# Kernel optimization log

Measured on AMD Instinct MI355X. Metric: run time of the kernel, lower is better.

Reference implementation:

```python
import jax, jax.numpy as jnp
import numpy as np

EPS = 1e-6

def masked_softmax(x, m, axis):
    # Faithful to KrantikariQA tensor_utils.masked_softmax:
    #   x = x*m; e = exp(x - max(x)) * m; e / (sum(e) + 1e-6)
    x = x * m
    ex = jnp.exp(x - jnp.max(x, axis=axis, keepdims=True)) * m
    return ex / (jnp.sum(ex, axis=axis, keepdims=True) + EPS)

def setup_inputs() -> dict:
    key = jax.random.key(0)
    k = jax.random.split(key, 7)
    Lq, Lp, B, D = 256, 256, 64, 1024
    q = jax.random.normal(k[0], (Lq, B, D), jnp.float32)
    p = jax.random.normal(k[1], (Lp, B, D), jnp.float32)
    qm = jax.random.randint(k[2], (B, Lq), 0, 2).astype(jnp.int32)
    pm = jax.random.randint(k[3], (B, Lp), 0, 2).astype(jnp.int32)
    # nn.Linear weights (out, in), no bias
    WF = jax.random.normal(k[4], (D, D), jnp.float32) * 0.02
    WG = jax.random.normal(k[5], (D, 2 * D), jnp.float32) * 0.02
    WH = jax.random.normal(k[6], (1, 2 * D), jnp.float32) * 0.02
    return {"q": q, "p": p, "qm": qm, "pm": pm, "WF": WF, "WG": WG, "WH": WH}

def reference(q, p, qm, pm, WF, WG, WH):
    # Attend: att = F(x), batch-first [B, L, D]
    att_q = jnp.einsum('lbd,ed->ble', q, WF)          # [B,Lq,D]
    att_p = jnp.einsum('lbd,ed->ble', p, WF)          # [B,Lp,D]
    e = jnp.einsum('bqe,bpe->bqp', att_q, att_p)      # [B,Lq,Lp]
    m = qm.astype(q.dtype)[:, :, None] * pm.astype(q.dtype)[:, None, :]  # [B,Lq,Lp]
    softmax_j = masked_softmax(e, m, axis=2)                              # over Lp
    softmax_i = masked_softmax(e.transpose(0, 2, 1), m.transpose(0, 2, 1), axis=2)  # [B,Lp,Lq]
    beta = jnp.einsum('bqp,pbd->bqd', softmax_j, p)   # [B,Lq,D]
    alpha = jnp.einsum('bpq,qbd->bpd', softmax_i, q)  # [B,Lp,D]
    # Compare
    v1 = jnp.concatenate([q.transpose(1, 0, 2), beta], axis=-1) @ WG.T   # [B,Lq,D]
    v2 = jnp.concatenate([p.transpose(1, 0, 2), alpha], axis=-1) @ WG.T  # [B,Lp,D]
    # Aggregate
    sum_v1 = jnp.sum(v1, axis=1)  # [B,D]
    sum_v2 = jnp.sum(v2, axis=1)  # [B,D]
    return jnp.concatenate([sum_v1, sum_v2], axis=-1) @ WH.T  # [B,1]
```

## Files before the change

kernel.cpp:

```cpp
#include <hip/hip_runtime.h>

typedef _Float16 f16x8 __attribute__((ext_vector_type(8)));
using f32x4 = __attribute__((ext_vector_type(4))) float;

constexpr int B = 64, L = 256, D = 1024;
constexpr int BD = B * D;
constexpr float EPS = 1e-6f;

__device__ __forceinline__ void gload_lds16(const void* g, void* l) {
    __builtin_amdgcn_global_load_lds((const __attribute__((address_space(1))) void*)g,
                                     (__attribute__((address_space(3))) void*)l,
                                     16, 0, 0);
}

__global__ __launch_bounds__(256) void k_cvt(const float* __restrict__ x,
                                             short* __restrict__ y) {
    const int i = blockIdx.x * 256 + threadIdx.x;
    const float4* xp = (const float4*)x;
    float4 a = xp[2 * i], b = xp[2 * i + 1];
    float v[8] = {a.x, a.y, a.z, a.w, b.x, b.y, b.z, b.w};
    union { _Float16 h[8]; int4 q; } u;
    #pragma unroll
    for (int k = 0; k < 8; ++k) u.h[k] = (_Float16)v[k];
    ((int4*)y)[i] = u.q;
}

__global__ __launch_bounds__(256) void k_cvt_t(const float* __restrict__ X,
                                               short* __restrict__ Y) {
    __shared__ float tile[32][33];
    const int t = threadIdx.x;
    const int rt = blockIdx.y, ct = blockIdx.x;
    const int r = t >> 3, c4 = (t & 7) * 4;
    float4 v = *(const float4*)(X + (long)(rt * 32 + r) * D + ct * 32 + c4);
    tile[r][c4] = v.x; tile[r][c4 + 1] = v.y; tile[r][c4 + 2] = v.z; tile[r][c4 + 3] = v.w;
    __syncthreads();
    union { _Float16 h[4]; short4 s; } u;
    u.h[0] = (_Float16)tile[c4 + 0][r];
    u.h[1] = (_Float16)tile[c4 + 1][r];
    u.h[2] = (_Float16)tile[c4 + 2][r];
    u.h[3] = (_Float16)tile[c4 + 3][r];
    *(short4*)(Y + (long)(ct * 32 + r) * D + rt * 32 + c4) = u.s;
}

__global__ __launch_bounds__(256, 4) void k_gemm16(
    const short* __restrict__ A, long strideA, long batchA,
    const short* __restrict__ Bm, long strideB, long batchB,
    int K, int bx, int per_batch, int f16_out,
    short* __restrict__ Ch, float* __restrict__ Cf, int ldC, long batchC)
{
    __shared__ __align__(16) short lds_s[16384];
    const int t = threadIdx.x, lane = t & 63, w = t >> 6;
    const int wm = w >> 1, wn = w & 1;

    const int lin = blockIdx.x;
    const int chunk = gridDim.x >> 3;
    const int swz = (lin & 7) * chunk + (lin >> 3);
    const int z = swz / per_batch;
    const int r0 = swz % per_batch;
    const int mb = (r0 / bx) * 128, nb = (r0 % bx) * 128;

    const char* mat = (w < 2) ? ((const char*)A + batchA * z)
                              : ((const char*)Bm + batchB * z);
    const long rstride = (w < 2) ? strideA : strideB;
    const int row0 = (w < 2) ? mb : nb;
    const int half = (w & 1) * 64;
    const char* sp[4];
    #pragma unroll
    for (int i = 0; i < 4; ++i) {
        int tr = half + i * 16 + (lane >> 2);
        int g = (lane & 3) ^ ((tr >> 1) & 3);
        sp[i] = mat + (long)(row0 + tr) * rstride + g * 16;
    }
    short* dst0 = lds_s + ((w >> 1) ? 4096 : 0) + (w & 1) * 2048;

    int aoff[4], boff[4];
    #pragma unroll
    for (int f = 0; f < 4; ++f) {
        int ra = wm * 64 + f * 16 + (lane & 15);
        aoff[f] = (ra * 4 + ((lane >> 4) ^ ((ra >> 1) & 3))) * 16;
        int rb = wn * 64 + f * 16 + (lane & 15);
        boff[f] = 8192 + (rb * 4 + ((lane >> 4) ^ ((rb >> 1) & 3))) * 16;
    }

    f32x4 acc[4][4] = {};
    const int NT = K >> 5;

    {
        #pragma unroll
        for (int i = 0; i < 4; ++i) gload_lds16(sp[i], dst0 + i * 512);
    }
    __syncthreads();

    int cur = 0;
    for (int kt = 0; kt < NT; ++kt) {
        if (kt + 1 < NT) {
            short* dst = dst0 + (cur ^ 1) * 8192;
            long ko = (long)(kt + 1) * 64;
            #pragma unroll
            for (int i = 0; i < 4; ++i) gload_lds16(sp[i] + ko, dst + i * 512);
        }
        const char* lb = (const char*)lds_s + cur * 16384;
        f16x8 a[4], b[4];
        #pragma unroll
        for (int f = 0; f < 4; ++f) {
            a[f] = *(const f16x8*)(lb + aoff[f]);
            b[f] = *(const f16x8*)(lb + boff[f]);
        }
        #pragma unroll
        for (int i = 0; i < 4; ++i)
            #pragma unroll
            for (int j = 0; j < 4; ++j)
                acc[i][j] = __builtin_amdgcn_mfma_f32_16x16x32_f16(b[j], a[i], acc[i][j], 0, 0, 0);
        __syncthreads();
        cur ^= 1;
    }

    const long zC = batchC * z;
    #pragma unroll
    for (int i = 0; i < 4; ++i)
        #pragma unroll
        for (int j = 0; j < 4; ++j) {
            int row = mb + wm * 64 + i * 16 + (lane & 15);
            int col = nb + wn * 64 + j * 16 + (lane >> 4) * 4;
            long idx = zC + (long)row * ldC + col;
            if (f16_out) {
                union { _Float16 h[4]; short4 s; } u;
                #pragma unroll
                for (int rr = 0; rr < 4; ++rr) u.h[rr] = (_Float16)acc[i][j][rr];
                *(short4*)(Ch + idx) = u.s;
            } else {
                float4 v = make_float4(acc[i][j][0], acc[i][j][1], acc[i][j][2], acc[i][j][3]);
                *(float4*)(Cf + idx) = v;
            }
        }
}

__global__ __launch_bounds__(256) void k_pass1(const float* __restrict__ E,
                                               const int* __restrict__ qm,
                                               const int* __restrict__ pm,
                                               float* __restrict__ impart,
                                               float* __restrict__ ispart,
                                               float* __restrict__ cjpart) {
    const int qc = blockIdx.x, b = blockIdx.y;
    const int p = threadIdx.x, lane = p & 63, w = p >> 6;
    const int q0 = qc * 32;
    __shared__ float wred[32][4];
    __shared__ float rowmx[32], rowsm[32], qmv_s[32];
    if (p < 32) qmv_s[p] = (float)qm[b * L + q0 + p];
    __syncthreads();
    const float pmv = (float)pm[b * L + p];
    const float* eb = E + b * (L * L) + q0 * L + p;

    float xv[32];
    float im = -1e30f;
    #pragma unroll
    for (int r = 0; r < 32; ++r) {
        float mm = pmv * qmv_s[r];
        float x = eb[r * L] * mm;
        xv[r] = x;
        im = fmaxf(im, x);
        float v = x;
        #pragma unroll
        for (int o = 32; o; o >>= 1) v = fmaxf(v, __shfl_xor(v, o));
        if (lane == 0) wred[r][w] = v;
    }
    __syncthreads();
    if (p < 32) rowmx[p] = fmaxf(fmaxf(wred[p][0], wred[p][1]), fmaxf(wred[p][2], wred[p][3]));
    __syncthreads();
    float is = 0.f;
    #pragma unroll
    for (int r = 0; r < 32; ++r) {
        float mm = pmv * qmv_s[r];
        is += mm * __expf(xv[r] - im);
        float v = mm * __expf(xv[r] - rowmx[r]);
        #pragma unroll
        for (int o = 32; o; o >>= 1) v += __shfl_xor(v, o);
        if (lane == 0) wred[r][w] = v;
    }
    __syncthreads();
    if (p < 32) rowsm[p] = wred[p][0] + wred[p][1] + wred[p][2] + wred[p][3];
    __syncthreads();
    float cj = 0.f;
    #pragma unroll
    for (int r = 0; r < 32; ++r) {
        float mm = pmv * qmv_s[r];
        cj += mm * __expf(xv[r] - rowmx[r]) / (rowsm[r] + EPS);
    }
    const int o = (b * 8 + qc) * 256 + p;
    impart[o] = im; ispart[o] = is; cjpart[o] = cj;
}

__global__ __launch_bounds__(256) void k_combine(const float* __restrict__ impart,
                                                 const float* __restrict__ ispart,
                                                 const float* __restrict__ cjpart,
                                                 float* __restrict__ rmi,
                                                 float* __restrict__ rsi,
                                                 float* __restrict__ colj) {
    const int b = blockIdx.x, p = threadIdx.x;
    const int base = b * 8 * 256 + p;
    float m = -1e30f, s = 0.f, c = 0.f;
    #pragma unroll
    for (int k = 0; k < 8; ++k) m = fmaxf(m, impart[base + k * 256]);
    #pragma unroll
    for (int k = 0; k < 8; ++k) {
        s += ispart[base + k * 256] * __expf(impart[base + k * 256] - m);
        c += cjpart[base + k * 256];
    }
    rmi[b * L + p] = m; rsi[b * L + p] = s; colj[b * L + p] = c;
}

__global__ __launch_bounds__(256) void k_colsum_i(const float* __restrict__ E,
                                                  const int* __restrict__ qm,
                                                  const int* __restrict__ pm,
                                                  const float* __restrict__ rmaxi,
                                                  const float* __restrict__ rsumi,
                                                  float* __restrict__ coli) {
    const int wid = threadIdx.x >> 6, lane = threadIdx.x & 63;
    const int row = blockIdx.x * 4 + wid;
    const int b = row >> 8;
    const float qmv = (float)qm[row];
    const float* er = E + row * L;
    float acc = 0.f;
    #pragma unroll
    for (int i = 0; i < 4; ++i) {
        int pp = lane + 64 * i;
        float mm = qmv * (float)pm[b * L + pp];
        float x = er[pp] * mm;
        acc += mm * __expf(x - rmaxi[b * L + pp]) / (rsumi[b * L + pp] + EPS);
    }
    #pragma unroll
    for (int o = 32; o; o >>= 1) acc += __shfl_xor(acc, o);
    if (lane == 0) coli[row] = acc;
}

__global__ __launch_bounds__(256) void k_sums(const short* __restrict__ Q16,
                                              const short* __restrict__ P16,
                                              const float* __restrict__ colj,
                                              const float* __restrict__ coli,
                                              float* __restrict__ sumq,
                                              float* __restrict__ sump,
                                              float* __restrict__ sumbeta,
                                              float* __restrict__ sumalpha) {
    const int b = blockIdx.x >> 2;
    const int d = (blockIdx.x & 3) * 256 + threadIdx.x;
    const _Float16* Q = (const _Float16*)Q16;
    const _Float16* P = (const _Float16*)P16;
    float aq = 0.f, ap = 0.f, ab = 0.f, aa = 0.f;
    for (int l = 0; l < L; ++l) {
        float qv = (float)Q[(long)l * BD + b * D + d];
        float pv = (float)P[(long)l * BD + b * D + d];
        aq += qv; ap += pv;
        ab += colj[b * L + l] * pv;
        aa += coli[b * L + l] * qv;
    }
    sumq[b * D + d] = aq;  sump[b * D + d] = ap;
    sumbeta[b * D + d] = ab; sumalpha[b * D + d] = aa;
}

__global__ __launch_bounds__(256) void k_gpart(const float* __restrict__ WG,
                                               const float* __restrict__ WH,
                                               float* __restrict__ gp1,
                                               float* __restrict__ gp2) {
    const int k = blockIdx.x * 256 + threadIdx.x;
    const int e0 = blockIdx.y * 128;
    float a = 0.f, c = 0.f;
    for (int e = 0; e < 128; ++e) {
        float w = WG[(long)(e0 + e) * (2 * D) + k];
        a += w * WH[e0 + e];
        c += w * WH[D + e0 + e];
    }
    gp1[blockIdx.y * 2048 + k] = a; gp2[blockIdx.y * 2048 + k] = c;
}

__global__ __launch_bounds__(256) void k_final(const float* __restrict__ sumq,
                                               const float* __restrict__ sump,
                                               const float* __restrict__ sumbeta,
                                               const float* __restrict__ sumalpha,
                                               const float* __restrict__ gp1,
                                               const float* __restrict__ gp2,
                                               float* __restrict__ out) {
    const int b = blockIdx.x, t = threadIdx.x;
    float acc = 0.f;
    for (int d = t; d < D; d += 256) {
        float g1d = 0.f, g1D = 0.f, g2d = 0.f, g2D = 0.f;
        #pragma unroll
        for (int ec = 0; ec < 8; ++ec) {
            g1d += gp1[ec * 2048 + d];     g1D += gp1[ec * 2048 + D + d];
            g2d += gp2[ec * 2048 + d];     g2D += gp2[ec * 2048 + D + d];
        }
        acc += sumq[b * D + d] * g1d + sumbeta[b * D + d] * g1D +
               sump[b * D + d] * g2d + sumalpha[b * D + d] * g2D;
    }
    #pragma unroll
    for (int o = 32; o; o >>= 1) acc += __shfl_xor(acc, o);
    __shared__ float red[4];
    const int wid = t >> 6, lane = t & 63;
    if (lane == 0) red[wid] = acc;
    __syncthreads();
    if (t == 0) out[b] = red[0] + red[1] + red[2] + red[3];
}

extern "C" void kernel_launch(void* const* d_in, const int* in_sizes, int n_in,
                              void* d_out, int out_size, void* d_ws, size_t ws_size,
                              hipStream_t stream) {
    const float* q  = (const float*)d_in[0];
    const float* p  = (const float*)d_in[1];
    const int*   qm = (const int*)d_in[2];
    const int*   pm = (const int*)d_in[3];
    const float* WF = (const float*)d_in[4];
    const float* WG = (const float*)d_in[5];
    const float* WH = (const float*)d_in[6];
    float* out = (float*)d_out;

    char* wsb = (char*)d_ws;
    short* q16   = (short*)(wsb);
    short* p16   = (short*)(wsb + (32l << 20));
    short* T16   = (short*)(wsb + (64l << 20));
    short* WFt16 = (short*)(wsb + (96l << 20));
    short* G16   = (short*)(wsb + (98l << 20));
    float* E     = (float*)(wsb + (100l << 20));
    float* st    = (float*)(wsb + (116l << 20));
    const int BL = B * L;
    float* impart = st;                 float* ispart = impart + B * 8 * 256;
    float* cjpart = ispart + B * 8 * 256;
    float* rmi  = cjpart + B * 8 * 256; float* rsi  = rmi + BL;
    float* colj = rsi + BL;             float* coli = colj + BL;
    float* sumq = coli + BL;            float* sump = sumq + B * D;
    float* sumb = sump + B * D;         float* suma = sumb + B * D;
    float* gp1  = suma + B * D;         float* gp2  = gp1 + 8 * 2048;

    k_cvt<<<8192, 256, 0, stream>>>(q, q16);
    k_cvt<<<8192, 256, 0, stream>>>(p, p16);
    k_cvt_t<<<dim3(32, 32), 256, 0, stream>>>(WF, WFt16);
    k_gemm16<<<64, 256, 0, stream>>>(WFt16, 2048, 0, WFt16, 2048, 0,
                                     1024, 8, 64, 1, G16, nullptr, 1024, 0);
    k_gemm16<<<1024, 256, 0, stream>>>(q16, 2048, 0, G16, 2048, 0,
                                       1024, 8, 1024, 1, T16, nullptr, 1024, 0);
    k_gemm16<<<256, 256, 0, stream>>>(T16, 64l * 2048, 2048, p16, 64l * 2048, 2048,
                                      1024, 2, 4, 0, nullptr, E, 256, 65536);
    k_pass1<<<dim3(8, B), 256, 0, stream>>>(E, qm, pm, impart, ispart, cjpart);
    k_combine<<<B, 256, 0, stream>>>(impart, ispart, cjpart, rmi, rsi, colj);
    k_colsum_i<<<BL / 4, 256, 0, stream>>>(E, qm, pm, rmi, rsi, coli);
    k_sums<<<B * 4, 256, 0, stream>>>(q16, p16, colj, coli, sumq, sump, sumb, suma);
    k_gpart<<<dim3(8, 8), 256, 0, stream>>>(WG, WH, gp1, gp2);
    k_final<<<B, 256, 0, stream>>>(sumq, sump, sumb, suma, gp1, gp2, out);
}
```

Baseline: 195.8 us.

## Templatize GEMM tiles, split-K WF^T WF, fuse conversions, split-L reduction sums

Replaces the fixed 128x128 GEMM with a templated version supporting different warp layouts, including a 256x256 tile for the big q·G GEMM. The GEMM also gets a single-barrier-per-iteration pipeline. The small WF^T·WF GEMM becomes a 4-way split-K with a fold kernel, giving more blocks. The q/p conversions are merged into one launch. The column-sum kernel is split over four L chunks with 8-wide vector loads, with the chunks reduced in the final kernel. This adds partial buffers and an extra fold launch.

```diff
diff --git a/kernel.cpp b/kernel.cpp
--- a/kernel.cpp
+++ b/kernel.cpp
@@ -13,16 +13,21 @@
                                      16, 0, 0);
 }
 
-__global__ __launch_bounds__(256) void k_cvt(const float* __restrict__ x,
-                                             short* __restrict__ y) {
+__global__ __launch_bounds__(256) void k_cvt2(const float* __restrict__ q,
+                                              const float* __restrict__ p,
+                                              short* __restrict__ q16,
+                                              short* __restrict__ p16) {
     const int i = blockIdx.x * 256 + threadIdx.x;
-    const float4* xp = (const float4*)x;
-    float4 a = xp[2 * i], b = xp[2 * i + 1];
+    constexpr int HALF = (L * B * D) / 8;
+    const float* src; short* dst; int j;
+    if (i < HALF) { src = q; dst = q16; j = i; }
+    else          { src = p; dst = p16; j = i - HALF; }
+    float4 a = ((const float4*)src)[2 * j], b = ((const float4*)src)[2 * j + 1];
     float v[8] = {a.x, a.y, a.z, a.w, b.x, b.y, b.z, b.w};
-    union { _Float16 h[8]; int4 q; } u;
+    union { _Float16 h[8]; int4 q4; } u;
     #pragma unroll
     for (int k = 0; k < 8; ++k) u.h[k] = (_Float16)v[k];
-    ((int4*)y)[i] = u.q;
+    ((int4*)dst)[j] = u.q4;
 }
 
 __global__ __launch_bounds__(256) void k_cvt_t(const float* __restrict__ X,
@@ -42,85 +47,97 @@
     *(short4*)(Y + (long)(ct * 32 + r) * D + rt * 32 + c4) = u.s;
 }
 
-__global__ __launch_bounds__(256, 4) void k_gemm16(
-    const short* __restrict__ A, long strideA, long batchA,
-    const short* __restrict__ Bm, long strideB, long batchB,
+template <int WM, int WN, int MR>
+__global__ __launch_bounds__(WM * WN * 64) void k_gemm(
+    const short* __restrict__ A, long sA, long bA,
+    const short* __restrict__ Bm, long sB, long bB,
     int K, int bx, int per_batch, int f16_out,
     short* __restrict__ Ch, float* __restrict__ Cf, int ldC, long batchC)
 {
-    __shared__ __align__(16) short lds_s[16384];
+    constexpr int BM = WM * MR * 16, BN = WN * 64;
+    constexpr int T = WM * WN * 64;
+    constexpr int TILEB = (BM + BN) * 64;
+    constexpr int ROUNDS = TILEB / (T * 16);
+    __shared__ __align__(16) char lds[2 * TILEB];
+
     const int t = threadIdx.x, lane = t & 63, w = t >> 6;
-    const int wm = w >> 1, wn = w & 1;
+    const int wm = w / WN, wn = w % WN;
 
     const int lin = blockIdx.x;
     const int chunk = gridDim.x >> 3;
     const int swz = (lin & 7) * chunk + (lin >> 3);
     const int z = swz / per_batch;
     const int r0 = swz % per_batch;
-    const int mb = (r0 / bx) * 128, nb = (r0 % bx) * 128;
-
-    const char* mat = (w < 2) ? ((const char*)A + batchA * z)
-                              : ((const char*)Bm + batchB * z);
-    const long rstride = (w < 2) ? strideA : strideB;
-    const int row0 = (w < 2) ? mb : nb;
-    const int half = (w & 1) * 64;
-    const char* sp[4];
-    #pragma unroll
-    for (int i = 0; i < 4; ++i) {
-        int tr = half + i * 16 + (lane >> 2);
-        int g = (lane & 3) ^ ((tr >> 1) & 3);
-        sp[i] = mat + (long)(row0 + tr) * rstride + g * 16;
-    }
-    short* dst0 = lds_s + ((w >> 1) ? 4096 : 0) + (w & 1) * 2048;
-
-    int aoff[4], boff[4];
-    #pragma unroll
-    for (int f = 0; f < 4; ++f) {
-        int ra = wm * 64 + f * 16 + (lane & 15);
-        aoff[f] = (ra * 4 + ((lane >> 4) ^ ((ra >> 1) & 3))) * 16;
-        int rb = wn * 64 + f * 16 + (lane & 15);
-        boff[f] = 8192 + (rb * 4 + ((lane >> 4) ^ ((rb >> 1) & 3))) * 16;
-    }
-
-    f32x4 acc[4][4] = {};
+    const int mb = (r0 / bx) * BM, nb = (r0 % bx) * BN;
+
+    const char* Ab = (const char*)A + bA * z;
+    const char* Bb = (const char*)Bm + bB * z;
+
+    const char* sp[ROUNDS];
+    #pragma unroll
+    for (int r = 0; r < ROUNDS; ++r) {
+        int g = r * T + t;
+        int row = g >> 2, sg = g & 3;
+        int lg = sg ^ ((row >> 1) & 3);
+        if (row < BM) sp[r] = Ab + (long)(mb + row) * sA + lg * 16;
+        else          sp[r] = Bb + (long)(nb + row - BM) * sB + lg * 16;
+    }
+
+    int aoff[MR], boff[4];
+    #pragma unroll
+    for (int i = 0; i < MR; ++i) {
+        int ra = wm * (MR * 16) + i * 16 + (lane & 15);
+        aoff[i] = ra * 64 + (((lane >> 4) ^ ((ra >> 1) & 3))) * 16;
+    }
+    #pragma unroll
+    for (int j = 0; j < 4; ++j) {
+        int rb = wn * 64 + j * 16 + (lane & 15);
+        boff[j] = BM * 64 + rb * 64 + (((lane >> 4) ^ ((rb >> 1) & 3))) * 16;
+    }
+
+    f32x4 acc[MR][4] = {};
     const int NT = K >> 5;
 
     {
         #pragma unroll
-        for (int i = 0; i < 4; ++i) gload_lds16(sp[i], dst0 + i * 512);
-    }
-    __syncthreads();
+        for (int r = 0; r < ROUNDS; ++r)
+            gload_lds16(sp[r], lds + (r * T + t) * 16);
+    }
 
     int cur = 0;
     for (int kt = 0; kt < NT; ++kt) {
+        asm volatile("s_waitcnt vmcnt(0)" ::: "memory");
+        __builtin_amdgcn_sched_barrier(0);
+        __builtin_amdgcn_s_barrier();
+        __builtin_amdgcn_sched_barrier(0);
         if (kt + 1 < NT) {
-            short* dst = dst0 + (cur ^ 1) * 8192;
-            long ko = (long)(kt + 1) * 64;
+            long kb = (long)(kt + 1) * 64;
+            char* dstb = lds + (cur ^ 1) * TILEB;
             #pragma unroll
-            for (int i = 0; i < 4; ++i) gload_lds16(sp[i] + ko, dst + i * 512);
-        }
-        const char* lb = (const char*)lds_s + cur * 16384;
-        f16x8 a[4], b[4];
-        #pragma unroll
-        for (int f = 0; f < 4; ++f) {
-            a[f] = *(const f16x8*)(lb + aoff[f]);
-            b[f] = *(const f16x8*)(lb + boff[f]);
-        }
-        #pragma unroll
-        for (int i = 0; i < 4; ++i)
+            for (int r = 0; r < ROUNDS; ++r)
+                gload_lds16(sp[r] + kb, dstb + (r * T + t) * 16);
+        }
+        __builtin_amdgcn_sched_barrier(0);
+        const char* lb = lds + cur * TILEB;
+        f16x8 fb[4], fa[MR];
+        #pragma unroll
+        for (int j = 0; j < 4; ++j) fb[j] = *(const f16x8*)(lb + boff[j]);
+        #pragma unroll
+        for (int i = 0; i < MR; ++i) fa[i] = *(const f16x8*)(lb + aoff[i]);
+        #pragma unroll
+        for (int i = 0; i < MR; ++i)
             #pragma unroll
             for (int j = 0; j < 4; ++j)
-                acc[i][j] = __builtin_amdgcn_mfma_f32_16x16x32_f16(b[j], a[i], acc[i][j], 0, 0, 0);
-        __syncthreads();
+                acc[i][j] = __builtin_amdgcn_mfma_f32_16x16x32_f16(fb[j], fa[i], acc[i][j], 0, 0, 0);
         cur ^= 1;
     }
 
     const long zC = batchC * z;
     #pragma unroll
-    for (int i = 0; i < 4; ++i)
+    for (int i = 0; i < MR; ++i)
         #pragma unroll
         for (int j = 0; j < 4; ++j) {
-            int row = mb + wm * 64 + i * 16 + (lane & 15);
+            int row = mb + wm * (MR * 16) + i * 16 + (lane & 15);
             int col = nb + wn * 64 + j * 16 + (lane >> 4) * 4;
             long idx = zC + (long)row * ldC + col;
             if (f16_out) {
@@ -133,6 +150,20 @@
                 *(float4*)(Cf + idx) = v;
             }
         }
+}
+
+__global__ __launch_bounds__(256) void k_fold_g(const float* __restrict__ Gp,
+                                                short* __restrict__ G16) {
+    const int i = blockIdx.x * 256 + threadIdx.x;
+    constexpr int N4 = (1 << 20) / 4;
+    const float4* g = (const float4*)Gp;
+    float4 v0 = g[i], v1 = g[N4 + i], v2 = g[2 * N4 + i], v3 = g[3 * N4 + i];
+    union { _Float16 h[4]; short4 s; } u;
+    u.h[0] = (_Float16)(v0.x + v1.x + v2.x + v3.x);
+    u.h[1] = (_Float16)(v0.y + v1.y + v2.y + v3.y);
+    u.h[2] = (_Float16)(v0.z + v1.z + v2.z + v3.z);
+    u.h[3] = (_Float16)(v0.w + v1.w + v2.w + v3.w);
+    ((short4*)G16)[i] = u.s;
 }
 
 __global__ __launch_bounds__(256) void k_pass1(const float* __restrict__ E,
@@ -233,28 +264,37 @@
     if (lane == 0) coli[row] = acc;
 }
 
-__global__ __launch_bounds__(256) void k_sums(const short* __restrict__ Q16,
-                                              const short* __restrict__ P16,
-                                              const float* __restrict__ colj,
-                                              const float* __restrict__ coli,
-                                              float* __restrict__ sumq,
-                                              float* __restrict__ sump,
-                                              float* __restrict__ sumbeta,
-                                              float* __restrict__ sumalpha) {
-    const int b = blockIdx.x >> 2;
-    const int d = (blockIdx.x & 3) * 256 + threadIdx.x;
-    const _Float16* Q = (const _Float16*)Q16;
-    const _Float16* P = (const _Float16*)P16;
-    float aq = 0.f, ap = 0.f, ab = 0.f, aa = 0.f;
-    for (int l = 0; l < L; ++l) {
-        float qv = (float)Q[(long)l * BD + b * D + d];
-        float pv = (float)P[(long)l * BD + b * D + d];
-        aq += qv; ap += pv;
-        ab += colj[b * L + l] * pv;
-        aa += coli[b * L + l] * qv;
-    }
-    sumq[b * D + d] = aq;  sump[b * D + d] = ap;
-    sumbeta[b * D + d] = ab; sumalpha[b * D + d] = aa;
+__global__ __launch_bounds__(128) void k_sums2(const short* __restrict__ Q16,
+                                               const short* __restrict__ P16,
+                                               const float* __restrict__ colj,
+                                               const float* __restrict__ coli,
+                                               float* __restrict__ pq,
+                                               float* __restrict__ pp,
+                                               float* __restrict__ pb,
+                                               float* __restrict__ pa) {
+    const int c = blockIdx.x, b = blockIdx.y, t = threadIdx.x;
+    const int d0 = t * 8;
+    float aq[8] = {}, ap[8] = {}, ab[8] = {}, aa[8] = {};
+    for (int l = c * 64; l < c * 64 + 64; ++l) {
+        union { int4 v; _Float16 h[8]; } uq, up;
+        uq.v = *(const int4*)(Q16 + (long)l * BD + b * D + d0);
+        up.v = *(const int4*)(P16 + (long)l * BD + b * D + d0);
+        float cj = colj[b * L + l], ci = coli[b * L + l];
+        #pragma unroll
+        for (int k = 0; k < 8; ++k) {
+            float qf = (float)uq.h[k], pf = (float)up.h[k];
+            aq[k] += qf; ap[k] += pf; ab[k] += cj * pf; aa[k] += ci * qf;
+        }
+    }
+    const long o = ((long)c * B + b) * D + d0;
+    *(float4*)(pq + o) = make_float4(aq[0], aq[1], aq[2], aq[3]);
+    *(float4*)(pq + o + 4) = make_float4(aq[4], aq[5], aq[6], aq[7]);
+    *(float4*)(pp + o) = make_float4(ap[0], ap[1], ap[2], ap[3]);
+    *(float4*)(pp + o + 4) = make_float4(ap[4], ap[5], ap[6], ap[7]);
+    *(float4*)(pb + o) = make_float4(ab[0], ab[1], ab[2], ab[3]);
+    *(float4*)(pb + o + 4) = make_float4(ab[4], ab[5], ab[6], ab[7]);
+    *(float4*)(pa + o) = make_float4(aa[0], aa[1], aa[2], aa[3]);
+    *(float4*)(pa + o + 4) = make_float4(aa[4], aa[5], aa[6], aa[7]);
 }
 
 __global__ __launch_bounds__(256) void k_gpart(const float* __restrict__ WG,
@@ -272,24 +312,29 @@
     gp1[blockIdx.y * 2048 + k] = a; gp2[blockIdx.y * 2048 + k] = c;
 }
 
-__global__ __launch_bounds__(256) void k_final(const float* __restrict__ sumq,
-                                               const float* __restrict__ sump,
-                                               const float* __restrict__ sumbeta,
-                                               const float* __restrict__ sumalpha,
-                                               const float* __restrict__ gp1,
-                                               const float* __restrict__ gp2,
-                                               float* __restrict__ out) {
+__global__ __launch_bounds__(256) void k_final2(const float* __restrict__ pq,
+                                                const float* __restrict__ pp,
+                                                const float* __restrict__ pb,
+                                                const float* __restrict__ pa,
+                                                const float* __restrict__ gp1,
+                                                const float* __restrict__ gp2,
+                                                float* __restrict__ out) {
     const int b = blockIdx.x, t = threadIdx.x;
     float acc = 0.f;
     for (int d = t; d < D; d += 256) {
+        float sq = 0.f, sp_ = 0.f, sb = 0.f, sa = 0.f;
+        #pragma unroll
+        for (int c2 = 0; c2 < 4; ++c2) {
+            long o = ((long)c2 * B + b) * D + d;
+            sq += pq[o]; sp_ += pp[o]; sb += pb[o]; sa += pa[o];
+        }
         float g1d = 0.f, g1D = 0.f, g2d = 0.f, g2D = 0.f;
         #pragma unroll
         for (int ec = 0; ec < 8; ++ec) {
             g1d += gp1[ec * 2048 + d];     g1D += gp1[ec * 2048 + D + d];
             g2d += gp2[ec * 2048 + d];     g2D += gp2[ec * 2048 + D + d];
         }
-        acc += sumq[b * D + d] * g1d + sumbeta[b * D + d] * g1D +
-               sump[b * D + d] * g2d + sumalpha[b * D + d] * g2D;
+        acc += sq * g1d + sb * g1D + sp_ * g2d + sa * g2D;
     }
     #pragma unroll
     for (int o = 32; o; o >>= 1) acc += __shfl_xor(acc, o);
@@ -318,30 +363,31 @@
     short* T16   = (short*)(wsb + (64l << 20));
     short* WFt16 = (short*)(wsb + (96l << 20));
     short* G16   = (short*)(wsb + (98l << 20));
+    float* Gp    = (float*)(wsb + (100l << 20));
     float* E     = (float*)(wsb + (100l << 20));
     float* st    = (float*)(wsb + (116l << 20));
     const int BL = B * L;
-    float* impart = st;                 float* ispart = impart + B * 8 * 256;
+    float* impart = st;                  float* ispart = impart + B * 8 * 256;
     float* cjpart = ispart + B * 8 * 256;
-    float* rmi  = cjpart + B * 8 * 256; float* rsi  = rmi + BL;
-    float* colj = rsi + BL;             float* coli = colj + BL;
-    float* sumq = coli + BL;            float* sump = sumq + B * D;
-    float* sumb = sump + B * D;         float* suma = sumb + B * D;
-    float* gp1  = suma + B * D;         float* gp2  = gp1 + 8 * 2048;
-
-    k_cvt<<<8192, 256, 0, stream>>>(q, q16);
-    k_cvt<<<8192, 256, 0, stream>>>(p, p16);
+    float* rmi  = cjpart + B * 8 * 256;  float* rsi  = rmi + BL;
+    float* colj = rsi + BL;              float* coli = colj + BL;
+    float* pq   = coli + BL;             float* pp   = pq + 4 * BD;
+    float* pb   = pp + 4 * BD;           float* pa   = pb + 4 * BD;
+    float* gp1  = pa + 4 * BD;           float* gp2  = gp1 + 8 * 2048;
+
+    k_cvt2<<<16384, 256, 0, stream>>>(q, p, q16, p16);
     k_cvt_t<<<dim3(32, 32), 256, 0, stream>>>(WF, WFt16);
-    k_gemm16<<<64, 256, 0, stream>>>(WFt16, 2048, 0, WFt16, 2048, 0,
-                                     1024, 8, 64, 1, G16, nullptr, 1024, 0);
-    k_gemm16<<<1024, 256, 0, stream>>>(q16, 2048, 0, G16, 2048, 0,
-                                       1024, 8, 1024, 1, T16, nullptr, 1024, 0);
-    k_gemm16<<<256, 256, 0, stream>>>(T16, 64l * 2048, 2048, p16, 64l * 2048, 2048,
-                                      1024, 2, 4, 0, nullptr, E, 256, 65536);
+    k_gemm<2, 2, 4><<<256, 256, 0, stream>>>(WFt16, 2048, 512, WFt16, 2048, 512,
+                                             256, 8, 64, 0, nullptr, Gp, 1024, 1l << 20);
+    k_fold_g<<<1024, 256, 0, stream>>>(Gp, G16);
+    k_gemm<2, 4, 8><<<256, 512, 0, stream>>>(q16, 2048, 0, G16, 2048, 0,
+                                             1024, 4, 256, 1, T16, nullptr, 1024, 0);
+    k_gemm<2, 2, 4><<<256, 256, 0, stream>>>(T16, 64l * 2048, 2048, p16, 64l * 2048, 2048,
+                                             1024, 2, 4, 0, nullptr, E, 256, 65536);
     k_pass1<<<dim3(8, B), 256, 0, stream>>>(E, qm, pm, impart, ispart, cjpart);
     k_combine<<<B, 256, 0, stream>>>(impart, ispart, cjpart, rmi, rsi, colj);
     k_colsum_i<<<BL / 4, 256, 0, stream>>>(E, qm, pm, rmi, rsi, coli);
-    k_sums<<<B * 4, 256, 0, stream>>>(q16, p16, colj, coli, sumq, sump, sumb, suma);
+    k_sums2<<<dim3(4, B), 128, 0, stream>>>(q16, p16, colj, coli, pq, pp, pb, pa);
     k_gpart<<<dim3(8, 8), 256, 0, stream>>>(WG, WH, gp1, gp2);
-    k_final<<<B, 256, 0, stream>>>(sumq, sump, sumb, suma, gp1, gp2, out);
-}
+    k_final2<<<B, 256, 0, stream>>>(pq, pp, pb, pa, gp1, gp2, out);
+}
```

After: 183.1 us. -6.5%, faster.
